# Kernel optimization log

Measured on AMD Instinct MI355X. Metric: run time of the kernel, lower is better.

The kernel has to match this reference:

```python
import jax, jax.numpy as jnp
import numpy as np

D_MODEL = 1024
H = 16          # n_heads (kv heads)
G = 2           # n_gqa_groups
DQ = 64         # d_queries
DV = 64         # d_values
MAXLEN = 2048
NSEG = 8
SEG = MAXLEN // NSEG  # 256
EPS = 1e-5
ROPE_THETA = 10000.0


def setup_inputs() -> dict:
    key = jax.random.key(0)
    ks = jax.random.split(key, 10)
    N = 8
    w = lambda k, sh: jax.random.normal(k, sh, dtype=jnp.float32) * 0.02
    return {
        "query_sequences": jax.random.normal(ks[0], (N, MAXLEN, D_MODEL), dtype=jnp.float32),
        "key_sequences": jax.random.normal(ks[1], (N, MAXLEN, D_MODEL), dtype=jnp.float32),
        "value_sequences": jax.random.normal(ks[2], (N, MAXLEN, D_MODEL), dtype=jnp.float32),
        "ln_w": jnp.ones((D_MODEL,), dtype=jnp.float32),
        "ln_b": jnp.zeros((D_MODEL,), dtype=jnp.float32),
        "Wq": w(ks[3], (G * H * DQ, D_MODEL)),
        "Wk": w(ks[4], (H * DQ, D_MODEL)),
        "Wv": w(ks[5], (H * DV, D_MODEL)),
        "Wo": w(ks[6], (D_MODEL, H * DV)),
        "Wkc": w(ks[7], (DQ, SEG * DQ)),
        "bkc": jnp.zeros((DQ,), dtype=jnp.float32),
        "Wvc": w(ks[8], (DV, SEG * DV)),
        "bvc": jnp.zeros((DV,), dtype=jnp.float32),
    }


def _layernorm(x, w, b):
    mu = x.mean(-1, keepdims=True)
    var = ((x - mu) ** 2).mean(-1, keepdims=True)
    return (x - mu) * jax.lax.rsqrt(var + EPS) * w + b


def _rope(x):
    # x: [..., seq, DQ]; full-dim interleaved RoPE (rotary-embedding-torch convention)
    seq = x.shape[-2]
    inv_freq = 1.0 / (ROPE_THETA ** (jnp.arange(0, DQ, 2, dtype=jnp.float32) / DQ))  # [DQ/2]
    ang = jnp.arange(seq, dtype=jnp.float32)[:, None] * inv_freq[None, :]            # [seq, DQ/2]
    ang = jnp.repeat(ang, 2, axis=-1)                                                # [seq, DQ]
    cos, sin = jnp.cos(ang), jnp.sin(ang)
    x2 = x.reshape(x.shape[:-1] + (DQ // 2, 2))
    xrot = jnp.stack([-x2[..., 1], x2[..., 0]], axis=-1).reshape(x.shape)
    return x * cos + xrot * sin


def _forward(query_sequences, key_sequences, value_sequences,
             ln_w, ln_b, Wq, Wk, Wv, Wo, Wkc, bkc, Wvc, bvc):
    N, t, _ = query_sequences.shape
    q = _layernorm(query_sequences, ln_w, ln_b)
    k = _layernorm(key_sequences, ln_w, ln_b)
    v = _layernorm(value_sequences, ln_w, ln_b)

    qh = (q @ Wq.T).reshape(N, t, G, H, DQ).transpose(0, 2, 3, 1, 4)  # [N,G,H,t,DQ]
    kh = (k @ Wk.T).reshape(N, t, H, DQ).transpose(0, 2, 1, 3)        # [N,H,T,DQ]
    vh = (v @ Wv.T).reshape(N, t, H, DV).transpose(0, 2, 1, 3)        # [N,H,T,DV]

    qh = _rope(qh)
    kh = _rope(kh)

    # split into NSEG segments along time; keep last 2 raw, compress the rest
    kseg = kh.reshape(N, H, NSEG, SEG, DQ)
    vseg = vh.reshape(N, H, NSEG, SEG, DV)
    recent_k = kseg[:, :, -2:].reshape(N, H, 2 * SEG, DQ)
    recent_v = vseg[:, :, -2:].reshape(N, H, 2 * SEG, DV)
    k_sum = jax.nn.elu(kseg[:, :, :-2].reshape(N, H, NSEG - 2, SEG * DQ) @ Wkc.T + bkc)  # [N,H,S-2,DQ]
    v_sum = jax.nn.elu(vseg[:, :, :-2].reshape(N, H, NSEG - 2, SEG * DV) @ Wvc.T + bvc)
    K = jnp.concatenate([k_sum, recent_k], axis=-2)  # [N,H,Tk,DQ], Tk = (NSEG-2) + 2*SEG
    V = jnp.concatenate([v_sum, recent_v], axis=-2)

    # NOTE: original einsum sums over the GQA group axis g
    attn = jnp.einsum('nghtq,nhTq->nhtT', qh, K) * (1.0 / DQ ** 0.5)
    attn = 30.0 * jnp.tanh(attn / 30.0)  # grok scaled attn

    Tk = K.shape[-2]
    causal = jnp.arange(Tk)[None, :] <= jnp.arange(t)[:, None]  # tril slice [t, Tk]
    attn = jnp.where(causal, attn, -jnp.inf)
    attn = jax.nn.softmax(attn, axis=-1)

    out = jnp.einsum('nhtT,nhTv->nhtv', attn, V)
    out = out.transpose(0, 2, 1, 3).reshape(N, t, H * DV)
    return out @ Wo.T


def reference(query_sequences, key_sequences, value_sequences,
              ln_w, ln_b, Wq, Wk, Wv, Wo, Wkc, bkc, Wvc, bvc):
    return _forward(query_sequences, key_sequences, value_sequences,
                    ln_w, ln_b, Wq, Wk, Wv, Wo, Wkc, bkc, Wvc, bvc)
```

## Files before the change

kernel.cpp:

```cpp
#include <hip/hip_runtime.h>
#include <stdint.h>

#define DEV static __device__ __forceinline__

typedef unsigned short u16;
typedef unsigned int u32;
typedef __attribute__((ext_vector_type(4))) float f32x4;
typedef __attribute__((ext_vector_type(8))) short bf16x8;

DEV float bf2f(u16 u) { u32 x = ((u32)u) << 16; float f; __builtin_memcpy(&f, &x, 4); return f; }
DEV u16 f2bf(float f) { u32 x; __builtin_memcpy(&x, &f, 4); x = x + 0x7fffu + ((x >> 16) & 1u); return (u16)(x >> 16); }
DEV float lo16(u32 p) { u32 x = p << 16; float f; __builtin_memcpy(&f, &x, 4); return f; }
DEV float hi16(u32 p) { u32 x = p & 0xffff0000u; float f; __builtin_memcpy(&f, &x, 4); return f; }
DEV u32 pack2(float a, float b) { return (u32)f2bf(a) | ((u32)f2bf(b) << 16); }

DEV u32 cvtpk(float lo, float hi) {
  u32 r; asm("v_cvt_pk_bf16_f32 %0, %1, %2" : "=v"(r) : "v"(lo), "v"(hi)); return r;
}
DEV bf16x8 pk8(f32x4 a, f32x4 b) {
  union { u32 u[4]; bf16x8 v; } x;
  x.u[0] = cvtpk(a[0], a[1]); x.u[1] = cvtpk(a[2], a[3]);
  x.u[2] = cvtpk(b[0], b[1]); x.u[3] = cvtpk(b[2], b[3]);
  return x.v;
}

DEV f32x4 mfma16(bf16x8 a, bf16x8 b, f32x4 c) {
  return __builtin_amdgcn_mfma_f32_16x16x32_bf16(a, b, c, 0, 0, 0);
}

DEV void gl_lds16(const u16* g, u16* l) {
  __builtin_amdgcn_global_load_lds((const __attribute__((address_space(1))) void*)g,
                                   (__attribute__((address_space(3))) void*)l, 16, 0, 0);
}

__global__ __launch_bounds__(256) void prep_wqe_kernel(const float* __restrict__ Wq, u16* __restrict__ out) {
  int id = blockIdx.x * 256 + threadIdx.x;
  float4 a = ((const float4*)Wq)[id];
  float4 b = ((const float4*)Wq)[id + 262144];
  ushort4 o; o.x = f2bf(a.x + b.x); o.y = f2bf(a.y + b.y); o.z = f2bf(a.z + b.z); o.w = f2bf(a.w + b.w);
  ((ushort4*)out)[id] = o;
}

__global__ __launch_bounds__(256) void cast_w_kernel(const float* __restrict__ src, u16* __restrict__ dst) {
  int id = blockIdx.x * 256 + threadIdx.x;
  float4 a = ((const float4*)src)[id];
  ushort4 o; o.x = f2bf(a.x); o.y = f2bf(a.y); o.z = f2bf(a.z); o.w = f2bf(a.w);
  ((ushort4*)dst)[id] = o;
}

__global__ __launch_bounds__(256) void rope_cs_kernel(float* __restrict__ cs) {
  int id = blockIdx.x * 256 + threadIdx.x;
  int t = id >> 5, i = id & 31;
  double ang = (double)t * pow(10000.0, -(double)(2 * i) / 64.0);
  cs[id * 2] = (float)cos(ang);
  cs[id * 2 + 1] = (float)sin(ang);
}

__global__ __launch_bounds__(256) void ln_kernel(const float* __restrict__ x, const float* __restrict__ w,
                                                 const float* __restrict__ b, u16* __restrict__ out) {
  int row = blockIdx.x, t = threadIdx.x;
  float4 v = ((const float4*)(x + (size_t)row * 1024))[t];
  float s = v.x + v.y + v.z + v.w;
  float s2 = v.x * v.x + v.y * v.y + v.z * v.z + v.w * v.w;
#pragma unroll
  for (int off = 32; off; off >>= 1) { s += __shfl_xor(s, off, 64); s2 += __shfl_xor(s2, off, 64); }
  __shared__ float red[8];
  if ((t & 63) == 0) { red[t >> 6] = s; red[4 + (t >> 6)] = s2; }
  __syncthreads();
  s = red[0] + red[1] + red[2] + red[3];
  s2 = red[4] + red[5] + red[6] + red[7];
  float mu = s * 0.0009765625f;
  float var = s2 * 0.0009765625f - mu * mu;
  float rstd = rsqrtf(var + 1e-5f);
  float4 wv = ((const float4*)w)[t];
  float4 bv = ((const float4*)b)[t];
  ushort4 o;
  o.x = f2bf((v.x - mu) * rstd * wv.x + bv.x);
  o.y = f2bf((v.y - mu) * rstd * wv.y + bv.y);
  o.z = f2bf((v.z - mu) * rstd * wv.z + bv.z);
  o.w = f2bf((v.w - mu) * rstd * wv.w + bv.w);
  *(ushort4*)(out + (size_t)row * 1024 + t * 4) = o;
}

template <int MODE>
__global__ __launch_bounds__(256, 2) void gemm_nt(const u16* __restrict__ A, const u16* __restrict__ B,
                                                  void* __restrict__ Cout, int M, int Nd, int K,
                                                  const float* __restrict__ cs) {
  __shared__ u16 As[8192], Bs[8192];
  int tid = threadIdx.x, lane = tid & 63, wv = tid >> 6;
  int l15 = lane & 15, lq = lane >> 4;
  int bm = blockIdx.x * 128, bn = blockIdx.y * 128;
  int wm = (wv >> 1) * 64, wn = (wv & 1) * 64;
  int srow_in = lane >> 3, sslot = lane & 7;
  f32x4 acc[4][4] = {};
  for (int k0 = 0; k0 < K; k0 += 64) {
    __syncthreads();
#pragma unroll
    for (int it = 0; it < 4; ++it) {
      int ia = wv * 4 + it;
      int row = ia * 8 + srow_in;
      int gc = sslot ^ (row & 7);
      gl_lds16(A + (size_t)(bm + row) * K + k0 + gc * 8, &As[ia * 512]);
      gl_lds16(B + (size_t)(bn + row) * K + k0 + gc * 8, &Bs[ia * 512]);
    }
    __syncthreads();
#pragma unroll
    for (int h = 0; h < 2; ++h) {
      bf16x8 af[4], bfr[4];
#pragma unroll
      for (int mt = 0; mt < 4; ++mt) {
        int r = wm + mt * 16 + l15;
        af[mt] = *(const bf16x8*)&As[r * 64 + (((h * 4 + lq) ^ (r & 7)) * 8)];
      }
#pragma unroll
      for (int nt = 0; nt < 4; ++nt) {
        int r = wn + nt * 16 + l15;
        bfr[nt] = *(const bf16x8*)&Bs[r * 64 + (((h * 4 + lq) ^ (r & 7)) * 8)];
      }
#pragma unroll
      for (int mt = 0; mt < 4; ++mt)
#pragma unroll
        for (int nt = 0; nt < 4; ++nt)
          acc[mt][nt] = mfma16(af[mt], bfr[nt], acc[mt][nt]);
    }
  }
#pragma unroll
  for (int mt = 0; mt < 4; ++mt)
#pragma unroll
    for (int nt = 0; nt < 4; ++nt)
#pragma unroll
      for (int i = 0; i < 4; ++i) {
        int row = bm + wm + mt * 16 + lq * 4 + i;
        int col = bn + wn + nt * 16 + l15;
        float x = acc[mt][nt][i];
        if (MODE == 1) {
          ((float*)Cout)[(size_t)row * Nd + col] = x;
        } else if (MODE == 0) {
          ((u16*)Cout)[(size_t)row * Nd + col] = f2bf(x);
        } else {
          float xp = __shfl_xor(x, 1, 64);
          int t = row & 2047;
          int i0 = (col & 63) >> 1;
          float2 csv = *(const float2*)(cs + ((size_t)t * 32 + i0) * 2);
          float r = (col & 1) ? (x * csv.x + xp * csv.y) : (x * csv.x - xp * csv.y);
          ((u16*)Cout)[(size_t)row * Nd + col] = f2bf(r);
        }
      }
}

__global__ __launch_bounds__(512) void compress_partial_kernel(
    const u16* __restrict__ kh, const u16* __restrict__ vh,
    const u16* __restrict__ wkcb, const u16* __restrict__ wvcb,
    float* __restrict__ part) {
  int mt = blockIdx.x, ksl = blockIdx.y, kv = blockIdx.z;
  const u16* src = kv ? vh : kh;
  const u16* W = kv ? wvcb : wkcb;
  int tid = threadIdx.x, lane = tid & 63, wv = tid >> 6;
  int l15 = lane & 15, lq = lane >> 4;
  int r = mt * 16 + l15;
  int nh = r / 6, s = r % 6;
  int n = nh >> 4, h = nh & 15;
  const u16* arow = src + ((size_t)(n * 2048 + s * 256)) * 1024 + h * 64;
  f32x4 acc[4] = {};
  int kbase = (ksl * 8 + wv) * 256;
#pragma unroll
  for (int ks = 0; ks < 8; ++ks) {
    int k0 = kbase + ks * 32;
    int tau = k0 >> 6, d0 = k0 & 63;
    bf16x8 a = *(const bf16x8*)(arow + (size_t)tau * 1024 + d0 + lq * 8);
#pragma unroll
    for (int nt = 0; nt < 4; ++nt) {
      bf16x8 b = *(const bf16x8*)(W + (size_t)(nt * 16 + l15) * 16384 + k0 + lq * 8);
      acc[nt] = mfma16(a, b, acc[nt]);
    }
  }
  __shared__ float red[8][16][68];
#pragma unroll
  for (int nt = 0; nt < 4; ++nt)
#pragma unroll
    for (int i = 0; i < 4; ++i)
      red[wv][lq * 4 + i][nt * 16 + l15] = acc[nt][i];
  __syncthreads();
  int row = tid >> 5, o0 = (tid & 31) * 2;
  float v0 = 0.f, v1 = 0.f;
#pragma unroll
  for (int w8 = 0; w8 < 8; ++w8) { v0 += red[w8][row][o0]; v1 += red[w8][row][o0 + 1]; }
  size_t base = ((size_t)(kv * 8 + ksl) * 768 + mt * 16 + row) * 64 + o0;
  part[base] = v0;
  part[base + 1] = v1;
}

__global__ __launch_bounds__(256) void compress_finalize_kernel(
    const float* __restrict__ part, const float* __restrict__ bkc, const float* __restrict__ bvc,
    u16* __restrict__ kp, u16* __restrict__ vtp) {
  int id = blockIdx.x * 256 + threadIdx.x;
  int kv = blockIdx.y;
  int r = id >> 6, o = id & 63;
  float v = kv ? bvc[o] : bkc[o];
#pragma unroll
  for (int s8 = 0; s8 < 8; ++s8) v += part[((size_t)(kv * 8 + s8) * 768 + r) * 64 + o];
  v = v > 0.f ? v : expm1f(v);
  int nh = r / 6, s = r % 6;
  if (kv) vtp[((size_t)nh * 64 + o) * 576 + s] = f2bf(v);
  else    kp[((size_t)nh * 576 + s) * 64 + o] = f2bf(v);
}

__global__ __launch_bounds__(256) void copy_recent_kernel(const u16* __restrict__ kh, const u16* __restrict__ vh,
                                                          u16* __restrict__ kp, u16* __restrict__ vtp) {
  int bid = blockIdx.x;
  if (bid < 2280) {
    int u = bid * 256 + threadIdx.x;
    int dq8 = u & 7; int rest = u >> 3; int Tm6 = rest % 570; int nh = rest / 570;
    if (nh >= 128) return;
    uint4 val = {0, 0, 0, 0};
    if (Tm6 < 512) {
      int n = nh >> 4, h = nh & 15;
      val = *(const uint4*)&kh[((size_t)(n * 2048 + 1536 + Tm6)) * 1024 + h * 64 + dq8 * 8];
    }
    *(uint4*)&kp[((size_t)nh * 576 + 6 + Tm6) * 64 + dq8 * 8] = val;
  } else {
    int u = (bid - 2280) * 256 + threadIdx.x;
    int d = u & 63; int rest = u >> 6; int tch = rest % 72; int nh = rest / 72;
    if (nh >= 128) return;
    int n = nh >> 4, h = nh & 15;
#pragma unroll
    for (int ii = 0; ii < 8; ++ii) {
      int T = tch * 8 + ii;
      if (T < 6) continue;
      u16 v = 0;
      if (T < 518) v = vh[((size_t)(n * 2048 + 1536 + (T - 6))) * 1024 + h * 64 + d];
      vtp[((size_t)nh * 64 + d) * 576 + T] = v;
    }
  }
}

__global__ __launch_bounds__(256) void attn_kernel(const u16* __restrict__ qc, const u16* __restrict__ Kp,
                                                   const u16* __restrict__ VTp, u16* __restrict__ ao) {
  int qt = blockIdx.x, h = blockIdx.y, n = blockIdx.z;
  int tid = threadIdx.x, lane = tid & 63, wv = tid >> 6;
  int l15 = lane & 15, lq = lane >> 4;
  __shared__ u16 KS[4096], VS[4096];
  __shared__ float PS[4][1088];
  int q0 = qt * 64 + wv * 16;
  const u16* qrowp = qc + ((size_t)(n * 2048 + q0 + l15)) * 1024 + h * 64;
  bf16x8 aq0 = *(const bf16x8*)(qrowp + lq * 8);
  bf16x8 aq1 = *(const bf16x8*)(qrowp + 32 + lq * 8);
  const u16* Kph = Kp + (size_t)(n * 16 + h) * 576 * 64;
  const u16* Vph = VTp + (size_t)(n * 16 + h) * 64 * 576;
  f32x4 oa[4] = {};
  float rs[4] = {0.f, 0.f, 0.f, 0.f};
  float* PSW = &PS[wv][0];
  const float C1 = 0.012022458674074693f;
  const float C2 = -86.56170245333781f;
  int nchunks = min(qt + 1, 9);
  int srow0 = tid >> 3, sq0 = tid & 7;
  int srow1 = (256 + tid) >> 3, sq1 = tid & 7;
  int ksw0 = srow0 * 64 + ((sq0 ^ (srow0 & 7)) * 8);
  int ksw1 = srow1 * 64 + ((sq1 ^ (srow1 & 7)) * 8);
  uint4 kr0, kr1, vr0, vr1;
  {
    kr0 = *(const uint4*)&Kph[(size_t)srow0 * 64 + sq0 * 8];
    kr1 = *(const uint4*)&Kph[(size_t)srow1 * 64 + sq1 * 8];
    vr0 = *(const uint4*)&Vph[(size_t)srow0 * 576 + sq0 * 8];
    vr1 = *(const uint4*)&Vph[(size_t)srow1 * 576 + sq1 * 8];
  }
  for (int tc = 0; tc < nchunks; ++tc) {
    __syncthreads();
    *(uint4*)&KS[ksw0] = kr0;
    *(uint4*)&KS[ksw1] = kr1;
    *(uint4*)&VS[ksw0] = vr0;
    *(uint4*)&VS[ksw1] = vr1;
    if (tc + 1 < nchunks) {
      int Tb = (tc + 1) * 64;
      kr0 = *(const uint4*)&Kph[(size_t)(Tb + srow0) * 64 + sq0 * 8];
      kr1 = *(const uint4*)&Kph[(size_t)(Tb + srow1) * 64 + sq1 * 8];
      vr0 = *(const uint4*)&Vph[(size_t)srow0 * 576 + Tb + sq0 * 8];
      vr1 = *(const uint4*)&Vph[(size_t)srow1 * 576 + Tb + sq1 * 8];
    }
    __syncthreads();
    f32x4 sv[4];
    __builtin_amdgcn_s_setprio(1);
#pragma unroll
    for (int tt = 0; tt < 4; ++tt) {
      int row = tt * 16 + l15, r7 = row & 7;
      bf16x8 b0 = *(const bf16x8*)&KS[row * 64 + ((lq ^ r7) * 8)];
      bf16x8 b1 = *(const bf16x8*)&KS[row * 64 + (((4 | lq) ^ r7) * 8)];
      f32x4 c = {0.f, 0.f, 0.f, 0.f};
      c = mfma16(aq0, b0, c);
      c = mfma16(aq1, b1, c);
      sv[tt] = c;
    }
    __builtin_amdgcn_s_setprio(0);
    float p[4][4];
    bool needmask = (tc == qt) || (tc == 8);
    if (needmask) {
      int qb = q0 + lq * 4;
      int Tbase = tc * 64;
#pragma unroll
      for (int tt = 0; tt < 4; ++tt) {
        int T = Tbase + tt * 16 + l15;
        bool tval = (T < 518);
#pragma unroll
        for (int i = 0; i < 4; ++i) {
          float e = __builtin_amdgcn_exp2f(sv[tt][i] * C1);
          float pe = __builtin_amdgcn_exp2f(C2 * __builtin_amdgcn_rcpf(e + 1.f));
          bool ok = tval && (T <= qb + i);
          pe = ok ? pe : 0.f;
          p[tt][i] = pe;
          rs[i] += pe;
        }
      }
    } else {
#pragma unroll
      for (int tt = 0; tt < 4; ++tt)
#pragma unroll
        for (int i = 0; i < 4; ++i) {
          float e = __builtin_amdgcn_exp2f(sv[tt][i] * C1);
          float pe = __builtin_amdgcn_exp2f(C2 * __builtin_amdgcn_rcpf(e + 1.f));
          p[tt][i] = pe;
          rs[i] += pe;
        }
    }
#pragma unroll
    for (int tt = 0; tt < 4; ++tt)
#pragma unroll
      for (int i = 0; i < 4; ++i)
        PSW[(lq * 4 + i) * 68 + tt * 16 + l15] = p[tt][i];
    const float* prow = PSW + l15 * 68;
    f32x4 r0a = *(const f32x4*)(prow + lq * 8);
    f32x4 r0b = *(const f32x4*)(prow + lq * 8 + 4);
    f32x4 r1a = *(const f32x4*)(prow + lq * 8 + 32);
    f32x4 r1b = *(const f32x4*)(prow + lq * 8 + 36);
    bf16x8 pa0 = pk8(r0a, r0b);
    bf16x8 pa1 = pk8(r1a, r1b);
    __builtin_amdgcn_s_setprio(1);
#pragma unroll
    for (int ct = 0; ct < 4; ++ct) {
      int row = ct * 16 + l15, r7 = row & 7;
      bf16x8 bv0 = *(const bf16x8*)&VS[row * 64 + ((lq ^ r7) * 8)];
      bf16x8 bv1 = *(const bf16x8*)&VS[row * 64 + (((4 | lq) ^ r7) * 8)];
      oa[ct] = mfma16(pa0, bv0, oa[ct]);
      oa[ct] = mfma16(pa1, bv1, oa[ct]);
    }
    __builtin_amdgcn_s_setprio(0);
  }
#pragma unroll
  for (int i = 0; i < 4; ++i)
#pragma unroll
    for (int off = 1; off < 16; off <<= 1) rs[i] += __shfl_xor(rs[i], off, 64);
  u16* aop = ao + ((size_t)(n * 2048)) * 1024 + h * 64;
#pragma unroll
  for (int i = 0; i < 4; ++i) {
    float inv = 1.0f / rs[i];
    int q = q0 + lq * 4 + i;
#pragma unroll
    for (int ct = 0; ct < 4; ++ct) {
      int dv = ct * 16 + l15;
      aop[(size_t)q * 1024 + dv] = f2bf(oa[ct][i] * inv);
    }
  }
}

extern "C" void kernel_launch(void* const* d_in, const int* in_sizes, int n_in,
                              void* d_out, int out_size, void* d_ws, size_t ws_size,
                              hipStream_t stream) {
  const float* q_in = (const float*)d_in[0];
  const float* k_in = (const float*)d_in[1];
  const float* v_in = (const float*)d_in[2];
  const float* ln_w = (const float*)d_in[3];
  const float* ln_b = (const float*)d_in[4];
  const float* Wq = (const float*)d_in[5];
  const float* Wk = (const float*)d_in[6];
  const float* Wv = (const float*)d_in[7];
  const float* Wo = (const float*)d_in[8];
  const float* Wkc = (const float*)d_in[9];
  const float* bkc = (const float*)d_in[10];
  const float* Wvc = (const float*)d_in[11];
  const float* bvc = (const float*)d_in[12];

  char* ws = (char*)d_ws;
  const size_t MB = 1u << 20;
  u16* wqe = (u16*)(ws + 0 * MB);
  u16* wkb = (u16*)(ws + 2 * MB);
  u16* wvb = (u16*)(ws + 4 * MB);
  u16* wob = (u16*)(ws + 6 * MB);
  u16* wkcb = (u16*)(ws + 8 * MB);
  u16* wvcb = (u16*)(ws + 10 * MB);
  float* csb = (float*)(ws + 12 * MB);
  u16* xn = (u16*)(ws + 13 * MB);
  float* partf = (float*)(ws + 13 * MB);
  u16* qcb = (u16*)(ws + 45 * MB);
  u16* khb = (u16*)(ws + 77 * MB);
  u16* vhb = (u16*)(ws + 109 * MB);
  u16* kp = (u16*)(ws + 141 * MB);
  u16* vtp = (u16*)(ws + 141 * MB + 9437184);
  u16* aob = khb;

  prep_wqe_kernel<<<1024, 256, 0, stream>>>(Wq, wqe);
  cast_w_kernel<<<1024, 256, 0, stream>>>(Wk, wkb);
  cast_w_kernel<<<1024, 256, 0, stream>>>(Wv, wvb);
  cast_w_kernel<<<1024, 256, 0, stream>>>(Wo, wob);
  cast_w_kernel<<<1024, 256, 0, stream>>>(Wkc, wkcb);
  cast_w_kernel<<<1024, 256, 0, stream>>>(Wvc, wvcb);
  rope_cs_kernel<<<256, 256, 0, stream>>>(csb);

  dim3 gg(128, 8);
  ln_kernel<<<16384, 256, 0, stream>>>(q_in, ln_w, ln_b, xn);
  gemm_nt<2><<<gg, 256, 0, stream>>>(xn, wqe, qcb, 16384, 1024, 1024, csb);
  ln_kernel<<<16384, 256, 0, stream>>>(k_in, ln_w, ln_b, xn);
  gemm_nt<2><<<gg, 256, 0, stream>>>(xn, wkb, khb, 16384, 1024, 1024, csb);
  ln_kernel<<<16384, 256, 0, stream>>>(v_in, ln_w, ln_b, xn);
  gemm_nt<0><<<gg, 256, 0, stream>>>(xn, wvb, vhb, 16384, 1024, 1024, csb);

  compress_partial_kernel<<<dim3(48, 8, 2), 512, 0, stream>>>(khb, vhb, wkcb, wvcb, partf);
  compress_finalize_kernel<<<dim3(192, 2), 256, 0, stream>>>(partf, bkc, bvc, kp, vtp);
  copy_recent_kernel<<<4584, 256, 0, stream>>>(khb, vhb, kp, vtp);
  attn_kernel<<<dim3(32, 16, 8), 256, 0, stream>>>(qcb, kp, vtp, aob);
  gemm_nt<1><<<gg, 256, 0, stream>>>(aob, wob, (float*)d_out, 16384, 1024, 1024, csb);
}
```

Baseline: 418.6 us.

## Process 128 queries per attention block to reuse K/V tiles across two m-subtiles

Each attention workgroup now handles 128 query rows (32 per wave, as two 16-row subtiles) instead of 64, so every K/V chunk staged in shared memory serves twice as many queries and the grid halves. The grid is also reordered so heads vary fastest. Waves skip chunks beyond their own causal diagonal, which leaves some waves idle inside a block and adds register pressure from doubled accumulators. Global K/V load traffic per query drops.

Result: no change. 426.6 us (+1.9%).

```diff
diff --git a/kernel.cpp b/kernel.cpp
--- a/kernel.cpp
+++ b/kernel.cpp
@@ -236,23 +236,28 @@
 
 __global__ __launch_bounds__(256) void attn_kernel(const u16* __restrict__ qc, const u16* __restrict__ Kp,
                                                    const u16* __restrict__ VTp, u16* __restrict__ ao) {
-  int qt = blockIdx.x, h = blockIdx.y, n = blockIdx.z;
+  int h = blockIdx.x, qt = blockIdx.y, n = blockIdx.z;
   int tid = threadIdx.x, lane = tid & 63, wv = tid >> 6;
   int l15 = lane & 15, lq = lane >> 4;
   __shared__ u16 KS[4096], VS[4096];
   __shared__ float PS[4][1088];
-  int q0 = qt * 64 + wv * 16;
-  const u16* qrowp = qc + ((size_t)(n * 2048 + q0 + l15)) * 1024 + h * 64;
-  bf16x8 aq0 = *(const bf16x8*)(qrowp + lq * 8);
-  bf16x8 aq1 = *(const bf16x8*)(qrowp + 32 + lq * 8);
+  int q0 = qt * 128 + wv * 32;
+  const u16* qr0 = qc + ((size_t)(n * 2048 + q0 + l15)) * 1024 + h * 64;
+  const u16* qr1 = qc + ((size_t)(n * 2048 + q0 + 16 + l15)) * 1024 + h * 64;
+  bf16x8 aq[2][2];
+  aq[0][0] = *(const bf16x8*)(qr0 + lq * 8);
+  aq[0][1] = *(const bf16x8*)(qr0 + 32 + lq * 8);
+  aq[1][0] = *(const bf16x8*)(qr1 + lq * 8);
+  aq[1][1] = *(const bf16x8*)(qr1 + 32 + lq * 8);
   const u16* Kph = Kp + (size_t)(n * 16 + h) * 576 * 64;
   const u16* Vph = VTp + (size_t)(n * 16 + h) * 64 * 576;
-  f32x4 oa[4] = {};
-  float rs[4] = {0.f, 0.f, 0.f, 0.f};
+  f32x4 oa[2][4] = {};
+  float rs[2][4] = {};
   float* PSW = &PS[wv][0];
   const float C1 = 0.012022458674074693f;
   const float C2 = -86.56170245333781f;
-  int nchunks = min(qt + 1, 9);
+  int nchunks = min(2 * qt + 2, 9);
+  int dc = 2 * qt + (wv >> 1);
   int srow0 = tid >> 3, sq0 = tid & 7;
   int srow1 = (256 + tid) >> 3, sq1 = tid & 7;
   int ksw0 = srow0 * 64 + ((sq0 ^ (srow0 & 7)) * 8);
@@ -278,87 +283,91 @@
       vr1 = *(const uint4*)&Vph[(size_t)srow1 * 576 + Tb + sq1 * 8];
     }
     __syncthreads();
-    f32x4 sv[4];
-    __builtin_amdgcn_s_setprio(1);
-#pragma unroll
-    for (int tt = 0; tt < 4; ++tt) {
-      int row = tt * 16 + l15, r7 = row & 7;
-      bf16x8 b0 = *(const bf16x8*)&KS[row * 64 + ((lq ^ r7) * 8)];
-      bf16x8 b1 = *(const bf16x8*)&KS[row * 64 + (((4 | lq) ^ r7) * 8)];
-      f32x4 c = {0.f, 0.f, 0.f, 0.f};
-      c = mfma16(aq0, b0, c);
-      c = mfma16(aq1, b1, c);
-      sv[tt] = c;
-    }
-    __builtin_amdgcn_s_setprio(0);
-    float p[4][4];
-    bool needmask = (tc == qt) || (tc == 8);
-    if (needmask) {
-      int qb = q0 + lq * 4;
-      int Tbase = tc * 64;
+    if (tc > dc) continue;
+    bool needmask = (tc == dc) || (tc == 8);
+    int Tbase = tc * 64;
+#pragma unroll
+    for (int ms = 0; ms < 2; ++ms) {
+      f32x4 sv[4];
+      __builtin_amdgcn_s_setprio(1);
 #pragma unroll
       for (int tt = 0; tt < 4; ++tt) {
-        int T = Tbase + tt * 16 + l15;
-        bool tval = (T < 518);
-#pragma unroll
-        for (int i = 0; i < 4; ++i) {
-          float e = __builtin_amdgcn_exp2f(sv[tt][i] * C1);
-          float pe = __builtin_amdgcn_exp2f(C2 * __builtin_amdgcn_rcpf(e + 1.f));
-          bool ok = tval && (T <= qb + i);
-          pe = ok ? pe : 0.f;
-          p[tt][i] = pe;
-          rs[i] += pe;
+        int row = tt * 16 + l15, r7 = row & 7;
+        bf16x8 b0 = *(const bf16x8*)&KS[row * 64 + ((lq ^ r7) * 8)];
+        bf16x8 b1 = *(const bf16x8*)&KS[row * 64 + (((4 | lq) ^ r7) * 8)];
+        f32x4 c = {0.f, 0.f, 0.f, 0.f};
+        c = mfma16(aq[ms][0], b0, c);
+        c = mfma16(aq[ms][1], b1, c);
+        sv[tt] = c;
+      }
+      __builtin_amdgcn_s_setprio(0);
+      float p[4][4];
+      if (needmask) {
+        int qb = q0 + ms * 16 + lq * 4;
+#pragma unroll
+        for (int tt = 0; tt < 4; ++tt) {
+          int T = Tbase + tt * 16 + l15;
+          bool tval = (T < 518);
+#pragma unroll
+          for (int i = 0; i < 4; ++i) {
+            float e = __builtin_amdgcn_exp2f(sv[tt][i] * C1);
+            float pe = __builtin_amdgcn_exp2f(C2 * __builtin_amdgcn_rcpf(e + 1.f));
+            bool ok = tval && (T <= qb + i);
+            pe = ok ? pe : 0.f;
+            p[tt][i] = pe;
+            rs[ms][i] += pe;
+          }
         }
-      }
-    } else {
+      } else {
+#pragma unroll
+        for (int tt = 0; tt < 4; ++tt)
+#pragma unroll
+          for (int i = 0; i < 4; ++i) {
+            float e = __builtin_amdgcn_exp2f(sv[tt][i] * C1);
+            float pe = __builtin_amdgcn_exp2f(C2 * __builtin_amdgcn_rcpf(e + 1.f));
+            p[tt][i] = pe;
+            rs[ms][i] += pe;
+          }
+      }
 #pragma unroll
       for (int tt = 0; tt < 4; ++tt)
 #pragma unroll
-        for (int i = 0; i < 4; ++i) {
-          float e = __builtin_amdgcn_exp2f(sv[tt][i] * C1);
-          float pe = __builtin_amdgcn_exp2f(C2 * __builtin_amdgcn_rcpf(e + 1.f));
-          p[tt][i] = pe;
-          rs[i] += pe;
-        }
-    }
-#pragma unroll
-    for (int tt = 0; tt < 4; ++tt)
-#pragma unroll
-      for (int i = 0; i < 4; ++i)
-        PSW[(lq * 4 + i) * 68 + tt * 16 + l15] = p[tt][i];
-    const float* prow = PSW + l15 * 68;
-    f32x4 r0a = *(const f32x4*)(prow + lq * 8);
-    f32x4 r0b = *(const f32x4*)(prow + lq * 8 + 4);
-    f32x4 r1a = *(const f32x4*)(prow + lq * 8 + 32);
-    f32x4 r1b = *(const f32x4*)(prow + lq * 8 + 36);
-    bf16x8 pa0 = pk8(r0a, r0b);
-    bf16x8 pa1 = pk8(r1a, r1b);
-    __builtin_amdgcn_s_setprio(1);
-#pragma unroll
-    for (int ct = 0; ct < 4; ++ct) {
-      int row = ct * 16 + l15, r7 = row & 7;
-      bf16x8 bv0 = *(const bf16x8*)&VS[row * 64 + ((lq ^ r7) * 8)];
-      bf16x8 bv1 = *(const bf16x8*)&VS[row * 64 + (((4 | lq) ^ r7) * 8)];
-      oa[ct] = mfma16(pa0, bv0, oa[ct]);
-      oa[ct] = mfma16(pa1, bv1, oa[ct]);
-    }
-    __builtin_amdgcn_s_setprio(0);
+        for (int i = 0; i < 4; ++i)
+          PSW[(lq * 4 + i) * 68 + tt * 16 + l15] = p[tt][i];
+      const float* prow = PSW + l15 * 68;
+      f32x4 r0a = *(const f32x4*)(prow + lq * 8);
+      f32x4 r0b = *(const f32x4*)(prow + lq * 8 + 4);
+      f32x4 r1a = *(const f32x4*)(prow + lq * 8 + 32);
+      f32x4 r1b = *(const f32x4*)(prow + lq * 8 + 36);
+      bf16x8 pa0 = pk8(r0a, r0b);
+      bf16x8 pa1 = pk8(r1a, r1b);
+      __builtin_amdgcn_s_setprio(1);
+#pragma unroll
+      for (int ct = 0; ct < 4; ++ct) {
+        int row = ct * 16 + l15, r7 = row & 7;
+        bf16x8 bv0 = *(const bf16x8*)&VS[row * 64 + ((lq ^ r7) * 8)];
+        bf16x8 bv1 = *(const bf16x8*)&VS[row * 64 + (((4 | lq) ^ r7) * 8)];
+        oa[ms][ct] = mfma16(pa0, bv0, oa[ms][ct]);
+        oa[ms][ct] = mfma16(pa1, bv1, oa[ms][ct]);
+      }
+      __builtin_amdgcn_s_setprio(0);
+    }
   }
-#pragma unroll
-  for (int i = 0; i < 4; ++i)
-#pragma unroll
-    for (int off = 1; off < 16; off <<= 1) rs[i] += __shfl_xor(rs[i], off, 64);
   u16* aop = ao + ((size_t)(n * 2048)) * 1024 + h * 64;
 #pragma unroll
-  for (int i = 0; i < 4; ++i) {
-    float inv = 1.0f / rs[i];
-    int q = q0 + lq * 4 + i;
-#pragma unroll
-    for (int ct = 0; ct < 4; ++ct) {
-      int dv = ct * 16 + l15;
-      aop[(size_t)q * 1024 + dv] = f2bf(oa[ct][i] * inv);
-    }
-  }
+  for (int ms = 0; ms < 2; ++ms)
+#pragma unroll
+    for (int i = 0; i < 4; ++i) {
+#pragma unroll
+      for (int off = 1; off < 16; off <<= 1) rs[ms][i] += __shfl_xor(rs[ms][i], off, 64);
+      float inv = 1.0f / rs[ms][i];
+      int q = q0 + ms * 16 + lq * 4 + i;
+#pragma unroll
+      for (int ct = 0; ct < 4; ++ct) {
+        int dv = ct * 16 + l15;
+        aop[(size_t)q * 1024 + dv] = f2bf(oa[ms][ct][i] * inv);
+      }
+    }
 }
 
 extern "C" void kernel_launch(void* const* d_in, const int* in_sizes, int n_in,
@@ -415,6 +424,6 @@
   compress_partial_kernel<<<dim3(48, 8, 2), 512, 0, stream>>>(khb, vhb, wkcb, wvcb, partf);
   compress_finalize_kernel<<<dim3(192, 2), 256, 0, stream>>>(partf, bkc, bvc, kp, vtp);
   copy_recent_kernel<<<4584, 256, 0, stream>>>(khb, vhb, kp, vtp);
-  attn_kernel<<<dim3(32, 16, 8), 256, 0, stream>>>(qcb, kp, vtp, aob);
+  attn_kernel<<<dim3(16, 16, 8), 256, 0, stream>>>(qcb, kp, vtp, aob);
   gemm_nt<1><<<gg, 256, 0, stream>>>(aob, wob, (float*)d_out, 16384, 1024, 1024, csb);
 }
```
